# Kernel optimization log

Measured on AMD Instinct MI355X. Metric: run time of the kernel, lower is better.

## Reference

```python
import jax, jax.numpy as jnp
import numpy as np

B, C, H, W = 8, 128, 128, 128
C5 = 5 * C


def setup_inputs() -> dict:
    key = jax.random.key(0)
    ks = jax.random.split(key, 9)
    s_dw = 0.1   # depthwise weight scale
    s_pw = 0.02  # pointwise weight scale
    return {
        "x": jax.random.normal(ks[0], (B, C, H, W), jnp.float32),
        "w1": jax.random.normal(ks[1], (C5, 1, 1, 1), jnp.float32) * s_dw,
        "b1": jax.random.normal(ks[2], (C5,), jnp.float32) * 0.01,
        "w2": jax.random.normal(ks[3], (C5, 1, 3, 3), jnp.float32) * s_dw,
        "b2": jax.random.normal(ks[4], (C5,), jnp.float32) * 0.01,
        "w3": jax.random.normal(ks[5], (C5, 1, 3, 3), jnp.float32) * s_dw,
        "b3": jax.random.normal(ks[6], (C5,), jnp.float32) * 0.01,
        "w4": jax.random.normal(ks[7], (C, C5, 1, 1), jnp.float32) * s_pw,
        "b4": jax.random.normal(ks[8], (C,), jnp.float32) * 0.01,
    }


def nnstacking(x):
    # pad H,W by 1 then stack the 4-neighborhood + center along channels -> 5C
    p = jnp.pad(x, ((0, 0), (0, 0), (1, 1), (1, 1)))
    return jnp.concatenate(
        [p[:, :, 2:, 1:-1],   # neighbor below (i+1, j)
         p[:, :, :-2, 1:-1],  # neighbor above (i-1, j)
         p[:, :, 1:-1, 2:],   # neighbor right (i, j+1)
         p[:, :, 1:-1, :-2],  # neighbor left  (i, j-1)
         p[:, :, 1:-1, 1:-1]],  # center
        axis=1)


def _conv(x, w, b, dilation, padding, groups):
    y = jax.lax.conv_general_dilated(
        x, w, window_strides=(1, 1),
        padding=[(padding, padding), (padding, padding)],
        rhs_dilation=(dilation, dilation),
        dimension_numbers=("NCHW", "OIHW", "NCHW"),
        feature_group_count=groups)
    return y + b[None, :, None, None]


def reference(x, w1, b1, w2, b2, w3, b3, w4, b4):
    shortcut = x
    s = nnstacking(x)  # (B, 5C, H, W)
    # three depthwise branches (groups = 5C): 1x1 rate-1, 3x3 dil-8, 3x3 dil-12
    y = (_conv(s, w1, b1, 1, 0, C5)
         + _conv(s, w2, b2, 8, 8, C5)
         + _conv(s, w3, b3, 12, 12, C5))
    # pointwise 5C -> C, then residual add
    return _conv(y, w4, b4, 1, 0, 1) + shortcut
```

## Files before the change

kernel.cpp:

```cpp
#include <hip/hip_runtime.h>
#include <stdint.h>
#include <stddef.h>


static constexpr int Cc  = 128;
static constexpr int C5  = 640;
static constexpr int Hh  = 128;
static constexpr int Ww  = 128;
static constexpr int LC  = 160;
static constexpr int GR  = 48;
static constexpr int PSz = GR * LC + 8;

typedef __attribute__((ext_vector_type(8))) short short8;
typedef __attribute__((ext_vector_type(4))) float f32x4;

__device__ __forceinline__ uint16_t f2bf(float f) {
  uint32_t b = __float_as_uint(f);
  b += 0x7fffu + ((b >> 16) & 1u);
  return (uint16_t)(b >> 16);
}
__device__ __forceinline__ float bflo(uint32_t v) { return __uint_as_float(v << 16); }
__device__ __forceinline__ float bfhi(uint32_t v) { return __uint_as_float(v & 0xffff0000u); }

__device__ __forceinline__ void async16(uint16_t* lds, const uint16_t* gm) {
  __builtin_amdgcn_global_load_lds(
      (const __attribute__((address_space(1))) uint32_t*)gm,
      (__attribute__((address_space(3))) uint32_t*)lds, 16, 0, 0);
}

__global__ void prep_kernel(const float* __restrict__ w1, const float* __restrict__ b1,
                            const float* __restrict__ w2, const float* __restrict__ b2,
                            const float* __restrict__ w3, const float* __restrict__ b3,
                            const float* __restrict__ w4,
                            uint16_t* __restrict__ w4b, float* __restrict__ cw2,
                            float* __restrict__ cw3, float* __restrict__ bsum) {
  int i = blockIdx.x * 256 + threadIdx.x;
  if (i < Cc * C5) w4b[i] = f2bf(w4[i]);
  if (i < C5) {
    bsum[i] = b1[i] + b2[i] + b3[i];
#pragma unroll
    for (int t = 0; t < 9; ++t) {
      float a = w2[i * 9 + t];
      if (t == 4) a += w1[i] + w3[i * 9 + 4];
      cw2[i * 9 + t] = a;
      cw3[i * 9 + t] = w3[i * 9 + t];
    }
  }
}

__global__ __launch_bounds__(256, 2) void dw_kernel(
    const float* __restrict__ x, const float* __restrict__ cw2,
    const float* __restrict__ cw3, const float* __restrict__ bsum,
    uint16_t* __restrict__ y, int b0) {
  __shared__ uint16_t xs[4 * PSz];

  const int band = blockIdx.x;
  const int g    = blockIdx.y;
  const int bl   = blockIdx.z;
  const int bb   = b0 + bl;
  const int i0   = band * 16;
  const int tid  = threadIdx.x;

#pragma unroll
  for (int it = 0; it < 30; ++it) {
    int idx  = it * 256 + tid;
    int col4 = idx % 40;
    int rr   = (idx / 40) % 48;
    int cel  = idx / 1920;
    int gi = i0 - 16 + rr;
    int gj = col4 * 4 - 16;
    float4 v = make_float4(0.f, 0.f, 0.f, 0.f);
    if ((unsigned)gi < 128u && col4 >= 4 && col4 < 36) {
      v = *(const float4*)(x + (((size_t)(bb * Cc + g * 4 + cel) * Hh + gi) << 7) + gj);
    }
    ushort4 h;
    h.x = f2bf(v.x); h.y = f2bf(v.y); h.z = f2bf(v.z); h.w = f2bf(v.w);
    *(ushort4*)(xs + cel * PSz + rr * LC + col4 * 4) = h;
  }
  __syncthreads();

  const int ce = tid & 3;
  const int jt = (tid >> 2) & 7;
  const int ir = tid >> 5;
  const int j0 = jt * 16;
  const int c  = g * 4 + ce;

  float rb[48];
#define LOAD_RB(ROW)                                                      \
  do {                                                                    \
    const uint16_t* _p = xs + ce * PSz + (ROW) * LC + j0;                 \
    _Pragma("unroll") for (int _u = 0; _u < 6; ++_u) {                    \
      uint4 _q = *(const uint4*)(_p + _u * 8);                            \
      rb[_u * 8 + 0] = bflo(_q.x); rb[_u * 8 + 1] = bfhi(_q.x);           \
      rb[_u * 8 + 2] = bflo(_q.y); rb[_u * 8 + 3] = bfhi(_q.y);           \
      rb[_u * 8 + 4] = bflo(_q.z); rb[_u * 8 + 5] = bfhi(_q.z);           \
      rb[_u * 8 + 6] = bflo(_q.w); rb[_u * 8 + 7] = bfhi(_q.w);           \
    }                                                                     \
  } while (0)

  {
    float w2r[3][9], w3r[3][9], bs[3];
    const int msA[3] = {4, 2, 3};
#pragma unroll
    for (int mi = 0; mi < 3; ++mi) {
      int k = msA[mi] * Cc + c;
#pragma unroll
      for (int t = 0; t < 9; ++t) {
        w2r[mi][t] = cw2[k * 9 + t];
        w3r[mi][t] = cw3[k * 9 + t];
      }
      bs[mi] = bsum[k];
    }

#pragma unroll
    for (int it2 = 0; it2 < 2; ++it2) {
      const int i     = i0 + ir + 8 * it2;
      const int rbase = ir + 8 * it2 + 16;
      float acc[3][16];
#pragma unroll
      for (int mi = 0; mi < 3; ++mi)
#pragma unroll
        for (int jj = 0; jj < 16; ++jj) acc[mi][jj] = bs[mi];

#define AROW3(DLT, WARR, UB, DD)                                          \
      do {                                                                \
        LOAD_RB(rbase + (DLT));                                           \
        _Pragma("unroll") for (int mi = 0; mi < 3; ++mi) {                \
          const int aj = (mi == 0) ? 0 : ((mi == 1) ? 1 : -1);            \
          _Pragma("unroll") for (int v = 0; v < 3; ++v) {                 \
            const float w = WARR[mi][(UB) + v];                           \
            const int e = 16 + (DD) * (v - 1) + aj;                       \
            _Pragma("unroll") for (int jj = 0; jj < 16; ++jj)             \
              acc[mi][jj] += w * rb[e + jj];                              \
          }                                                               \
        }                                                                 \
      } while (0)

      AROW3(-12, w3r, 0, 12);
      if (j0 == 0)   acc[1][11] -= w3r[1][0] * rb[16];
      if (j0 == 112) acc[2][4]  -= w3r[2][2] * rb[31];

      AROW3(-8, w2r, 0, 8);
      if (j0 == 0)   acc[1][7]  -= w2r[1][0] * rb[16];
      if (j0 == 112) acc[2][8]  -= w2r[2][2] * rb[31];

      {
        LOAD_RB(rbase);
#pragma unroll
        for (int mi = 0; mi < 3; ++mi) {
          const int aj = (mi == 0) ? 0 : ((mi == 1) ? 1 : -1);
#pragma unroll
          for (int v = 0; v < 3; ++v) {
            const float w = w2r[mi][3 + v];
            const int e = 16 + 8 * (v - 1) + aj;
#pragma unroll
            for (int jj = 0; jj < 16; ++jj) acc[mi][jj] += w * rb[e + jj];
          }
          {
            const float w = w3r[mi][3]; const int e = 4 + aj;
#pragma unroll
            for (int jj = 0; jj < 16; ++jj) acc[mi][jj] += w * rb[e + jj];
          }
          {
            const float w = w3r[mi][5]; const int e = 28 + aj;
#pragma unroll
            for (int jj = 0; jj < 16; ++jj) acc[mi][jj] += w * rb[e + jj];
          }
        }
        if (j0 == 0)   { acc[1][7] -= w2r[1][3] * rb[16]; acc[1][11] -= w3r[1][3] * rb[16]; }
        if (j0 == 112) { acc[2][8] -= w2r[2][5] * rb[31]; acc[2][4]  -= w3r[2][5] * rb[31]; }
      }

      AROW3(8, w2r, 6, 8);
      if (j0 == 0)   acc[1][7]  -= w2r[1][6] * rb[16];
      if (j0 == 112) acc[2][8]  -= w2r[2][8] * rb[31];

      AROW3(12, w3r, 6, 12);
      if (j0 == 0)   acc[1][11] -= w3r[1][6] * rb[16];
      if (j0 == 112) acc[2][4]  -= w3r[2][8] * rb[31];
#undef AROW3

#pragma unroll
      for (int mi = 0; mi < 3; ++mi) {
        const int msA_[3] = {4, 2, 3};
        int k4 = msA_[mi] * 32 + g;
        size_t base = (((size_t)(bl * 160 + k4) << 14) + (size_t)i * Ww + j0) * 4 + ce;
#pragma unroll
        for (int jj = 0; jj < 16; ++jj) y[base + jj * 4] = f2bf(acc[mi][jj]);
      }
    }
  }

  {
    float w2r[2][9], w3r[2][9], bs[2];
#pragma unroll
    for (int mi = 0; mi < 2; ++mi) {
      int k = mi * Cc + c;
#pragma unroll
      for (int t = 0; t < 9; ++t) {
        w2r[mi][t] = cw2[k * 9 + t];
        w3r[mi][t] = cw3[k * 9 + t];
      }
      bs[mi] = bsum[k];
    }

#pragma unroll
    for (int it2 = 0; it2 < 2; ++it2) {
      const int i     = i0 + ir + 8 * it2;
      const int rbase = ir + 8 * it2 + 16;
      float acc[2][16];
#pragma unroll
      for (int mi = 0; mi < 2; ++mi)
#pragma unroll
        for (int jj = 0; jj < 16; ++jj) acc[mi][jj] = bs[mi];

#define BROW3(MI, DLT, WARR, UB, DD, BADROW)                              \
      do {                                                                \
        LOAD_RB(rbase + (DLT));                                           \
        const float sel = ((i + (DLT)) == (BADROW)) ? 0.f : 1.f;          \
        _Pragma("unroll") for (int v = 0; v < 3; ++v) {                   \
          const float w = WARR[MI][(UB) + v] * sel;                       \
          const int e = 16 + (DD) * (v - 1);                              \
          _Pragma("unroll") for (int jj = 0; jj < 16; ++jj)               \
            acc[MI][jj] += w * rb[e + jj];                                \
        }                                                                 \
      } while (0)

#define BROWC(MI, DLT, BADROW)                                            \
      do {                                                                \
        LOAD_RB(rbase + (DLT));                                           \
        const float sel = ((i + (DLT)) == (BADROW)) ? 0.f : 1.f;          \
        _Pragma("unroll") for (int v = 0; v < 3; ++v) {                   \
          const float w = w2r[MI][3 + v] * sel;                           \
          const int e = 16 + 8 * (v - 1);                                 \
          _Pragma("unroll") for (int jj = 0; jj < 16; ++jj)               \
            acc[MI][jj] += w * rb[e + jj];                                \
        }                                                                 \
        {                                                                 \
          const float w = w3r[MI][3] * sel;                               \
          _Pragma("unroll") for (int jj = 0; jj < 16; ++jj)               \
            acc[MI][jj] += w * rb[4 + jj];                                \
        }                                                                 \
        {                                                                 \
          const float w = w3r[MI][5] * sel;                               \
          _Pragma("unroll") for (int jj = 0; jj < 16; ++jj)               \
            acc[MI][jj] += w * rb[28 + jj];                               \
        }                                                                 \
      } while (0)

      BROW3(0, -11, w3r, 0, 12, 0);
      BROW3(0, -7,  w2r, 0, 8, 0);
      BROWC(0, 1, 0);
      BROW3(0, 9,   w2r, 6, 8, 0);
      BROW3(0, 13,  w3r, 6, 12, 0);
      BROW3(1, -13, w3r, 0, 12, 127);
      BROW3(1, -9,  w2r, 0, 8, 127);
      BROWC(1, -1, 127);
      BROW3(1, 7,   w2r, 6, 8, 127);
      BROW3(1, 11,  w3r, 6, 12, 127);
#undef BROW3
#undef BROWC

#pragma unroll
      for (int mi = 0; mi < 2; ++mi) {
        int k4 = mi * 32 + g;
        size_t base = (((size_t)(bl * 160 + k4) << 14) + (size_t)i * Ww + j0) * 4 + ce;
#pragma unroll
        for (int jj = 0; jj < 16; ++jj) y[base + jj * 4] = f2bf(acc[mi][jj]);
      }
    }
  }
#undef LOAD_RB
}

__global__ __launch_bounds__(256, 2) void gemm_kernel(
    const uint16_t* __restrict__ w4b, const uint16_t* __restrict__ y,
    const float* __restrict__ x, const float* __restrict__ b4,
    float* __restrict__ out, int b0) {
  __shared__ uint16_t As[128 * 64];
  __shared__ uint16_t Bs[16 * 128 * 4];

  const int tid  = threadIdx.x;
  const int lane = tid & 63;
  const int wave = tid >> 6;
  const int p0   = blockIdx.x * 128;
  const int bl   = blockIdx.y;
  const int bb   = b0 + bl;

  const int col = lane & 15;
  const int q   = lane >> 4;
  const int o_base = (wave >> 1) * 64;
  const int p_base = (wave & 1) * 64;

  f32x4 acc[4][4];
#pragma unroll
  for (int fm = 0; fm < 4; ++fm)
#pragma unroll
    for (int fn = 0; fn < 4; ++fn) acc[fm][fn] = (f32x4){0.f, 0.f, 0.f, 0.f};

  for (int kt = 0; kt < 10; ++kt) {
#pragma unroll
    for (int l = 0; l < 4; ++l) {
      int u  = (wave * 4 + l) * 64 + lane;
      int o  = u >> 3, ch = u & 7;
      async16(As + u * 8, w4b + (size_t)o * 640 + kt * 64 + ch * 8);
    }
#pragma unroll
    for (int l = 0; l < 4; ++l) {
      int k4t = wave * 4 + l;
      async16(Bs + (k4t * 64 + lane) * 8,
              y + (((size_t)(bl * 160 + kt * 16 + k4t) << 14) + p0) * 4 + lane * 8);
    }
    __syncthreads();

#pragma unroll
    for (int kk = 0; kk < 2; ++kk) {
      short8 af[4], bf[4];
#pragma unroll
      for (int fm = 0; fm < 4; ++fm) {
        int o = o_base + fm * 16 + col;
        af[fm] = *(const short8*)(As + o * 64 + kk * 32 + q * 8);
      }
#pragma unroll
      for (int fn = 0; fn < 4; ++fn) {
        int p = p_base + fn * 16 + col;
        union { short8 s; uint32_t u[4]; } bu;
        const uint32_t* lo = (const uint32_t*)(Bs + ((kk * 8 + 2 * q) * 128 + p) * 4);
        const uint32_t* hi = (const uint32_t*)(Bs + ((kk * 8 + 2 * q + 1) * 128 + p) * 4);
        bu.u[0] = lo[0]; bu.u[1] = lo[1]; bu.u[2] = hi[0]; bu.u[3] = hi[1];
        bf[fn] = bu.s;
      }
#pragma unroll
      for (int fm = 0; fm < 4; ++fm)
#pragma unroll
        for (int fn = 0; fn < 4; ++fn)
          acc[fm][fn] = __builtin_amdgcn_mfma_f32_16x16x32_bf16(af[fm], bf[fn], acc[fm][fn], 0, 0, 0);
    }
    __syncthreads();
  }

#pragma unroll
  for (int fm = 0; fm < 4; ++fm) {
#pragma unroll
    for (int fn = 0; fn < 4; ++fn) {
      int pg = p0 + p_base + fn * 16 + col;
#pragma unroll
      for (int r = 0; r < 4; ++r) {
        int oo = o_base + fm * 16 + q * 4 + r;
        size_t oi = ((size_t)(bb * 128 + oo) << 14) + pg;
        out[oi] = acc[fm][fn][r] + b4[oo] + x[oi];
      }
    }
  }
}

extern "C" void kernel_launch(void* const* d_in, const int* in_sizes, int n_in,
                              void* d_out, int out_size, void* d_ws, size_t ws_size,
                              hipStream_t stream) {
  const float* x  = (const float*)d_in[0];
  const float* w1 = (const float*)d_in[1];
  const float* b1 = (const float*)d_in[2];
  const float* w2 = (const float*)d_in[3];
  const float* b2 = (const float*)d_in[4];
  const float* w3 = (const float*)d_in[5];
  const float* b3 = (const float*)d_in[6];
  const float* w4 = (const float*)d_in[7];
  const float* b4 = (const float*)d_in[8];
  float* out = (float*)d_out;

  char* ws = (char*)d_ws;
  uint16_t* w4b  = (uint16_t*)ws;
  float*    cw2  = (float*)(ws + 163840);
  float*    cw3  = (float*)(ws + 186880);
  float*    bsum = (float*)(ws + 209920);
  uint16_t* y    = (uint16_t*)(ws + (1 << 20));

  const size_t per_b = (size_t)160 * 16384 * 4 * 2;
  int nbc = 4;
  while (nbc > 1 && (size_t)(1 << 20) + (size_t)nbc * per_b > ws_size) nbc >>= 1;

  hipLaunchKernelGGL(prep_kernel, dim3(320), dim3(256), 0, stream,
                     w1, b1, w2, b2, w3, b3, w4, w4b, cw2, cw3, bsum);
  for (int b0 = 0; b0 < 8; b0 += nbc) {
    int nb = (8 - b0) < nbc ? (8 - b0) : nbc;
    hipLaunchKernelGGL(dw_kernel, dim3(8, 32, nb), dim3(256), 0, stream,
                       x, cw2, cw3, bsum, y, b0);
    hipLaunchKernelGGL(gemm_kernel, dim3(128, nb), dim3(256), 0, stream,
                       w4b, y, x, b4, out, b0);
  }
}
```

Baseline: 339.7 us.

## Restructure depthwise tiling, intermediate layout, and double-buffer GEMM loads

```diff
diff --git a/kernel.cpp b/kernel.cpp
--- a/kernel.cpp
+++ b/kernel.cpp
@@ -5,11 +5,9 @@
 
 static constexpr int Cc  = 128;
 static constexpr int C5  = 640;
-static constexpr int Hh  = 128;
-static constexpr int Ww  = 128;
-static constexpr int LC  = 160;
-static constexpr int GR  = 48;
-static constexpr int PSz = GR * LC + 8;
+static constexpr int LC2 = 160;
+static constexpr int NR2 = 58;
+static constexpr int PS2 = NR2 * LC2 + 8;
 
 typedef __attribute__((ext_vector_type(8))) short short8;
 typedef __attribute__((ext_vector_type(4))) float f32x4;
@@ -27,15 +25,27 @@
       (const __attribute__((address_space(1))) uint32_t*)gm,
       (__attribute__((address_space(3))) uint32_t*)lds, 16, 0, 0);
 }
+__device__ __forceinline__ void async16w(uint32_t* lds, const uint32_t* gm) {
+  __builtin_amdgcn_global_load_lds(
+      (const __attribute__((address_space(1))) uint32_t*)gm,
+      (__attribute__((address_space(3))) uint32_t*)lds, 16, 0, 0);
+}
 
 __global__ void prep_kernel(const float* __restrict__ w1, const float* __restrict__ b1,
                             const float* __restrict__ w2, const float* __restrict__ b2,
                             const float* __restrict__ w3, const float* __restrict__ b3,
                             const float* __restrict__ w4,
-                            uint16_t* __restrict__ w4b, float* __restrict__ cw2,
+                            uint16_t* __restrict__ w4s, float* __restrict__ cw2,
                             float* __restrict__ cw3, float* __restrict__ bsum) {
   int i = blockIdx.x * 256 + threadIdx.x;
-  if (i < Cc * C5) w4b[i] = f2bf(w4[i]);
+  if (i < Cc * C5) {
+    int e  = i & 7;
+    int o  = (i >> 3) & 127;
+    int ch = (i >> 10) & 7;
+    int kt = i >> 13;
+    int k  = kt * 64 + ch * 8 + e;
+    w4s[i] = f2bf(w4[o * 640 + k]);
+  }
   if (i < C5) {
     bsum[i] = b1[i] + b2[i] + b3[i];
 #pragma unroll
@@ -48,47 +58,51 @@
   }
 }
 
-__global__ __launch_bounds__(256, 2) void dw_kernel(
+__global__ __launch_bounds__(256, 4) void dw_kernel(
     const float* __restrict__ x, const float* __restrict__ cw2,
     const float* __restrict__ cw3, const float* __restrict__ bsum,
-    uint16_t* __restrict__ y, int b0) {
-  __shared__ uint16_t xs[4 * PSz];
+    uint32_t* __restrict__ yw, int b0) {
+  __shared__ uint16_t xs[2 * PS2];
 
   const int band = blockIdx.x;
   const int g    = blockIdx.y;
   const int bl   = blockIdx.z;
   const int bb   = b0 + bl;
-  const int i0   = band * 16;
+  const int i0   = band * 32;
   const int tid  = threadIdx.x;
 
 #pragma unroll
-  for (int it = 0; it < 30; ++it) {
-    int idx  = it * 256 + tid;
-    int col4 = idx % 40;
-    int rr   = (idx / 40) % 48;
-    int cel  = idx / 1920;
-    int gi = i0 - 16 + rr;
-    int gj = col4 * 4 - 16;
-    float4 v = make_float4(0.f, 0.f, 0.f, 0.f);
-    if ((unsigned)gi < 128u && col4 >= 4 && col4 < 36) {
-      v = *(const float4*)(x + (((size_t)(bb * Cc + g * 4 + cel) * Hh + gi) << 7) + gj);
-    }
-    ushort4 h;
-    h.x = f2bf(v.x); h.y = f2bf(v.y); h.z = f2bf(v.z); h.w = f2bf(v.w);
-    *(ushort4*)(xs + cel * PSz + rr * LC + col4 * 4) = h;
+  for (int it = 0; it < 19; ++it) {
+    int idx = it * 256 + tid;
+    if (idx < 4640) {
+      int cel  = idx / 2320;
+      int rem  = idx - cel * 2320;
+      int rr   = rem / 40;
+      int col4 = rem - rr * 40;
+      int gi = i0 - 13 + rr;
+      int gj = col4 * 4 - 16;
+      float4 v = make_float4(0.f, 0.f, 0.f, 0.f);
+      if ((unsigned)gi < 128u && col4 >= 4 && col4 < 36) {
+        v = *(const float4*)(x + (((size_t)(bb * Cc + 2 * g + cel)) << 14) + (gi << 7) + gj);
+      }
+      ushort4 h;
+      h.x = f2bf(v.x); h.y = f2bf(v.y); h.z = f2bf(v.z); h.w = f2bf(v.w);
+      *(ushort4*)(xs + cel * PS2 + rr * LC2 + col4 * 4) = h;
+    }
   }
   __syncthreads();
 
-  const int ce = tid & 3;
-  const int jt = (tid >> 2) & 7;
-  const int ir = tid >> 5;
+  const int ce = tid & 1;
+  const int jt = (tid >> 1) & 7;
+  const int ir = tid >> 4;
   const int j0 = jt * 16;
-  const int c  = g * 4 + ce;
+  const int c  = 2 * g + ce;
+  const int swz = ((g >> 2) & 3) << 3;
 
   float rb[48];
 #define LOAD_RB(ROW)                                                      \
   do {                                                                    \
-    const uint16_t* _p = xs + ce * PSz + (ROW) * LC + j0;                 \
+    const uint16_t* _p = xs + ce * PS2 + (ROW) * LC2 + j0;                \
     _Pragma("unroll") for (int _u = 0; _u < 6; ++_u) {                    \
       uint4 _q = *(const uint4*)(_p + _u * 8);                            \
       rb[_u * 8 + 0] = bflo(_q.x); rb[_u * 8 + 1] = bfhi(_q.x);           \
@@ -98,6 +112,28 @@
     }                                                                     \
   } while (0)
 
+#define STORE16(ACC, MVAL)                                                \
+  do {                                                                    \
+    uint32_t d0[8];                                                       \
+    _Pragma("unroll") for (int _k = 0; _k < 8; ++_k)                      \
+      d0[_k] = (uint32_t)f2bf(ACC[2 * _k]) |                              \
+               ((uint32_t)f2bf(ACC[2 * _k + 1]) << 16);                   \
+    uint32_t t0[4];                                                       \
+    _Pragma("unroll") for (int _k = 0; _k < 4; ++_k)                      \
+      t0[_k] = (uint32_t)__shfl_xor((int)(ce ? d0[_k] : d0[4 + _k]), 1, 64); \
+    uint32_t F[8];                                                        \
+    _Pragma("unroll") for (int _u = 0; _u < 4; ++_u) {                    \
+      uint32_t _a = ce ? t0[_u] : d0[_u];                                 \
+      uint32_t _b = ce ? d0[4 + _u] : t0[_u];                             \
+      F[2 * _u]     = (_a & 0xffffu) | (_b << 16);                        \
+      F[2 * _u + 1] = (_a >> 16) | (_b & 0xffff0000u);                    \
+    }                                                                     \
+    uint32_t* _dst = yw + (((size_t)(bl * 320 + (MVAL) * 64 + g)) << 14)  \
+                     + ((size_t)i << 7) + ((j0 + ce * 8) ^ swz);          \
+    *(uint4*)(_dst)     = make_uint4(F[0], F[1], F[2], F[3]);             \
+    *(uint4*)(_dst + 4) = make_uint4(F[4], F[5], F[6], F[7]);             \
+  } while (0)
+
   {
     float w2r[3][9], w3r[3][9], bs[3];
     const int msA[3] = {4, 2, 3};
@@ -114,8 +150,8 @@
 
 #pragma unroll
     for (int it2 = 0; it2 < 2; ++it2) {
-      const int i     = i0 + ir + 8 * it2;
-      const int rbase = ir + 8 * it2 + 16;
+      const int i     = i0 + ir + 16 * it2;
+      const int rbase = ir + 16 * it2 + 13;
       float acc[3][16];
 #pragma unroll
       for (int mi = 0; mi < 3; ++mi)
@@ -180,14 +216,9 @@
       if (j0 == 112) acc[2][4]  -= w3r[2][8] * rb[31];
 #undef AROW3
 
-#pragma unroll
-      for (int mi = 0; mi < 3; ++mi) {
-        const int msA_[3] = {4, 2, 3};
-        int k4 = msA_[mi] * 32 + g;
-        size_t base = (((size_t)(bl * 160 + k4) << 14) + (size_t)i * Ww + j0) * 4 + ce;
-#pragma unroll
-        for (int jj = 0; jj < 16; ++jj) y[base + jj * 4] = f2bf(acc[mi][jj]);
-      }
+      STORE16(acc[0], 4);
+      STORE16(acc[1], 2);
+      STORE16(acc[2], 3);
     }
   }
 
@@ -206,8 +237,8 @@
 
 #pragma unroll
     for (int it2 = 0; it2 < 2; ++it2) {
-      const int i     = i0 + ir + 8 * it2;
-      const int rbase = ir + 8 * it2 + 16;
+      const int i     = i0 + ir + 16 * it2;
+      const int rbase = ir + 16 * it2 + 13;
       float acc[2][16];
 #pragma unroll
       for (int mi = 0; mi < 2; ++mi)
@@ -261,24 +292,20 @@
 #undef BROW3
 #undef BROWC
 
-#pragma unroll
-      for (int mi = 0; mi < 2; ++mi) {
-        int k4 = mi * 32 + g;
-        size_t base = (((size_t)(bl * 160 + k4) << 14) + (size_t)i * Ww + j0) * 4 + ce;
-#pragma unroll
-        for (int jj = 0; jj < 16; ++jj) y[base + jj * 4] = f2bf(acc[mi][jj]);
-      }
+      STORE16(acc[0], 0);
+      STORE16(acc[1], 1);
     }
   }
 #undef LOAD_RB
+#undef STORE16
 }
 
 __global__ __launch_bounds__(256, 2) void gemm_kernel(
-    const uint16_t* __restrict__ w4b, const uint16_t* __restrict__ y,
+    const uint16_t* __restrict__ w4s, const uint32_t* __restrict__ y,
     const float* __restrict__ x, const float* __restrict__ b4,
     float* __restrict__ out, int b0) {
-  __shared__ uint16_t As[128 * 64];
-  __shared__ uint16_t Bs[16 * 128 * 4];
+  __shared__ uint16_t As[2][128 * 64];
+  __shared__ uint32_t Bs[2][32 * 128];
 
   const int tid  = threadIdx.x;
   const int lane = tid & 63;
@@ -298,45 +325,52 @@
 #pragma unroll
     for (int fn = 0; fn < 4; ++fn) acc[fm][fn] = (f32x4){0.f, 0.f, 0.f, 0.f};
 
+  auto stage = [&](int kt, int bufi) {
+#pragma unroll
+    for (int l = 0; l < 4; ++l) {
+      int u = (wave * 4 + l) * 64 + lane;
+      async16(&As[bufi][u * 8], w4s + kt * 8192 + u * 8);
+    }
+#pragma unroll
+    for (int l = 0; l < 4; ++l) {
+      int u   = (wave * 4 + l) * 64 + lane;
+      int k2l = u >> 5, pu = u & 31;
+      async16w(&Bs[bufi][u * 4],
+               y + (((size_t)(bl * 320 + kt * 32 + k2l)) << 14) + p0 + pu * 4);
+    }
+  };
+
+  stage(0, 0);
   for (int kt = 0; kt < 10; ++kt) {
-#pragma unroll
-    for (int l = 0; l < 4; ++l) {
-      int u  = (wave * 4 + l) * 64 + lane;
-      int o  = u >> 3, ch = u & 7;
-      async16(As + u * 8, w4b + (size_t)o * 640 + kt * 64 + ch * 8);
-    }
-#pragma unroll
-    for (int l = 0; l < 4; ++l) {
-      int k4t = wave * 4 + l;
-      async16(Bs + (k4t * 64 + lane) * 8,
-              y + (((size_t)(bl * 160 + kt * 16 + k4t) << 14) + p0) * 4 + lane * 8);
-    }
     __syncthreads();
-
+    if (kt < 9) stage(kt + 1, (kt + 1) & 1);
+    const int bufi = kt & 1;
+    const uint16_t* A = As[bufi];
+    const uint32_t* B = Bs[bufi];
 #pragma unroll
     for (int kk = 0; kk < 2; ++kk) {
-      short8 af[4], bf[4];
+      short8 af[4], bfr[4];
 #pragma unroll
       for (int fm = 0; fm < 4; ++fm) {
         int o = o_base + fm * 16 + col;
-        af[fm] = *(const short8*)(As + o * 64 + kk * 32 + q * 8);
+        af[fm] = *(const short8*)(A + (((kk * 4 + q) * 128) + o) * 8);
       }
 #pragma unroll
       for (int fn = 0; fn < 4; ++fn) {
-        int p = p_base + fn * 16 + col;
+        int pl  = p_base + fn * 16 + col;
+        int pls = pl ^ (q << 3);
         union { short8 s; uint32_t u[4]; } bu;
-        const uint32_t* lo = (const uint32_t*)(Bs + ((kk * 8 + 2 * q) * 128 + p) * 4);
-        const uint32_t* hi = (const uint32_t*)(Bs + ((kk * 8 + 2 * q + 1) * 128 + p) * 4);
-        bu.u[0] = lo[0]; bu.u[1] = lo[1]; bu.u[2] = hi[0]; bu.u[3] = hi[1];
-        bf[fn] = bu.s;
+#pragma unroll
+        for (int i2 = 0; i2 < 4; ++i2)
+          bu.u[i2] = B[(kk * 16 + q * 4 + i2) * 128 + pls];
+        bfr[fn] = bu.s;
       }
 #pragma unroll
       for (int fm = 0; fm < 4; ++fm)
 #pragma unroll
         for (int fn = 0; fn < 4; ++fn)
-          acc[fm][fn] = __builtin_amdgcn_mfma_f32_16x16x32_bf16(af[fm], bf[fn], acc[fm][fn], 0, 0, 0);
-    }
-    __syncthreads();
+          acc[fm][fn] = __builtin_amdgcn_mfma_f32_16x16x32_bf16(af[fm], bfr[fn], acc[fm][fn], 0, 0, 0);
+    }
   }
 
 #pragma unroll
@@ -369,23 +403,23 @@
   float* out = (float*)d_out;
 
   char* ws = (char*)d_ws;
-  uint16_t* w4b  = (uint16_t*)ws;
+  uint16_t* w4s  = (uint16_t*)ws;
   float*    cw2  = (float*)(ws + 163840);
   float*    cw3  = (float*)(ws + 186880);
   float*    bsum = (float*)(ws + 209920);
-  uint16_t* y    = (uint16_t*)(ws + (1 << 20));
-
-  const size_t per_b = (size_t)160 * 16384 * 4 * 2;
+  uint32_t* y    = (uint32_t*)(ws + (1 << 20));
+
+  const size_t per_b = (size_t)320 * 16384 * 4;
   int nbc = 4;
   while (nbc > 1 && (size_t)(1 << 20) + (size_t)nbc * per_b > ws_size) nbc >>= 1;
 
   hipLaunchKernelGGL(prep_kernel, dim3(320), dim3(256), 0, stream,
-                     w1, b1, w2, b2, w3, b3, w4, w4b, cw2, cw3, bsum);
+                     w1, b1, w2, b2, w3, b3, w4, w4s, cw2, cw3, bsum);
   for (int b0 = 0; b0 < 8; b0 += nbc) {
     int nb = (8 - b0) < nbc ? (8 - b0) : nbc;
-    hipLaunchKernelGGL(dw_kernel, dim3(8, 32, nb), dim3(256), 0, stream,
+    hipLaunchKernelGGL(dw_kernel, dim3(4, 64, nb), dim3(256), 0, stream,
                        x, cw2, cw3, bsum, y, b0);
     hipLaunchKernelGGL(gemm_kernel, dim3(128, nb), dim3(256), 0, stream,
-                       w4b, y, x, b4, out, b0);
-  }
-}
+                       w4s, y, x, b4, out, b0);
+  }
+}
```

Result: slower. 834.8 us (+145.8%).
